# Kernel tuning notes

Hardware: AMD Instinct MI355X
Metric: run time of the kernel (lower is better)

Reference implementation:

```python
import jax, jax.numpy as jnp
import numpy as np

B, LB, LC, H = 8, 512, 128, 256
H2 = 2 * H
MIN_WS, N_WIN = 5, 4


def _highway(x, Wn, bn, Wl, bl, Wg, bg):
    # AllenNLP-style highway: per layer, gate * relu(nonlinear) + (1-gate) * linear
    # Wn/Wl/Wg: [L, D, D]; bn/bl/bg: [L, D]
    for i in range(Wn.shape[0]):
        g = jax.nn.sigmoid(x @ Wg[i] + bg[i])
        x = g * jax.nn.relu(x @ Wn[i] + bn[i]) + (1.0 - g) * (x @ Wl[i] + bl[i])
    return x


def _additive_scores(q, k, Wq, bq, Wk, v):
    # 'BilinearAttention' in the repo is additive: v^T tanh(Wq q + Wk k)
    # q: [..., Lq, D], k: [..., Lk, D] -> scores [..., Lq, Lk]
    wq = q @ Wq + bq
    uh = k @ Wk
    return jnp.tanh(wq[..., :, None, :] + uh[..., None, :, :]) @ v


def setup_inputs() -> dict:
    key = jax.random.key(0)
    ks = jax.random.split(key, 32)
    s2 = 1.0 / np.sqrt(H2)
    s1 = 1.0 / np.sqrt(H)
    d = {
        'b_enc_output': jax.random.normal(ks[0], (B, LB, H), jnp.float32),
        'c_enc_output': jax.random.normal(ks[1], (B, LC, H), jnp.float32),
        'c_state': jax.random.normal(ks[2], (B, 1, H), jnp.float32),
        'b_mask': jnp.ones((B, LB), bool),
        'c_mask': jnp.ones((B, LC), bool),
    }
    # b_highway / c_highway: 2 layers, each with nonlinear/linear/gate Linear(2H,2H)
    for pfx, base in (('bh', 3), ('ch', 9)):
        d[pfx + '_Wn'] = jax.random.normal(ks[base + 0], (2, H2, H2), jnp.float32) * s2
        d[pfx + '_bn'] = jnp.zeros((2, H2), jnp.float32)
        d[pfx + '_Wl'] = jax.random.normal(ks[base + 1], (2, H2, H2), jnp.float32) * s2
        d[pfx + '_bl'] = jnp.zeros((2, H2), jnp.float32)
        d[pfx + '_Wg'] = jax.random.normal(ks[base + 2], (2, H2, H2), jnp.float32) * s2
        d[pfx + '_bg'] = jnp.zeros((2, H2), jnp.float32)
    # match_attn (2H) and area_attn (H)
    d['m_Wq'] = jax.random.normal(ks[15], (H2, H2), jnp.float32) * s2
    d['m_bq'] = jnp.zeros((H2,), jnp.float32)
    d['m_Wk'] = jax.random.normal(ks[16], (H2, H2), jnp.float32) * s2
    d['m_v'] = jax.random.normal(ks[17], (H2,), jnp.float32) * s2
    d['a_Wq'] = jax.random.normal(ks[18], (H, H), jnp.float32) * s1
    d['a_bq'] = jnp.zeros((H,), jnp.float32)
    d['a_Wk'] = jax.random.normal(ks[19], (H, H), jnp.float32) * s1
    d['a_v'] = jax.random.normal(ks[20], (H,), jnp.float32) * s1
    return d


def reference(b_enc_output, c_enc_output, c_state,
              bh_Wn, bh_bn, bh_Wl, bh_bl, bh_Wg, bh_bg,
              ch_Wn, ch_bn, ch_Wl, ch_bl, ch_Wg, ch_bg,
              m_Wq, m_bq, m_Wk, m_v,
              a_Wq, a_bq, a_Wk, a_v,
              b_mask, c_mask):
    Bsz, Lb, Hd = b_enc_output.shape
    Lc = c_enc_output.shape[1]
    # match(): highway over [enc ; c_state]
    cs_b = jnp.broadcast_to(c_state, (Bsz, Lb, Hd))
    cs_c = jnp.broadcast_to(c_state, (Bsz, Lc, Hd))
    b = _highway(jnp.concatenate([b_enc_output, cs_b], -1), bh_Wn, bh_bn, bh_Wl, bh_bl, bh_Wg, bh_bg)
    c = _highway(jnp.concatenate([c_enc_output, cs_c], -1), ch_Wn, ch_bn, ch_Wl, ch_bl, ch_Wg, ch_bg)
    m = _additive_scores(b, c, m_Wq, m_bq, m_Wk, m_v)  # [B,Lb,Lc]
    m = jnp.where(c_mask[:, None, :], m, -jnp.inf)
    b_score = jnp.where(b_mask, jnp.max(m, axis=-1), 0.0)  # [B,Lb]
    # segments(): multi-scale sliding windows (unfold) + area attention
    q = c_state[:, :, None, :]  # [B,1,1,H]
    segs, scores = [], []
    for i in range(N_WIN):
        ws = MIN_WS * (i + 1)
        n_seg = (Lb - ws) // MIN_WS + 1
        idx = jnp.arange(n_seg)[:, None] * MIN_WS + jnp.arange(ws)[None, :]  # [n_seg, ws]
        bw = b_enc_output[:, idx, :]  # [B,n_seg,ws,H]
        attn = jax.nn.softmax(_additive_scores(q, bw, a_Wq, a_bq, a_Wk, a_v), axis=-1)  # [B,n_seg,1,ws]
        segs.append(jnp.einsum('bnqw,bnwh->bnh', attn, bw))
        scores.append(b_score[:, idx].sum(-1))  # [B,n_seg]
    segments = jnp.concatenate(segs, axis=1)          # [B,N,H]
    s_score = jax.nn.softmax(jnp.concatenate(scores, axis=1), axis=-1)  # [B,N]
    out = jnp.einsum('bn,bnh->bh', s_score, segments)[:, None, :]  # [B,1,H]
    return out, s_score, b_score
```

## Files before the change

kernel.cpp:

```cpp
#include <hip/hip_runtime.h>
#include <hip/hip_bf16.h>
#include <cstdint>
#include <cstddef>


typedef unsigned short ushort8 __attribute__((ext_vector_type(8)));
typedef float f32x4 __attribute__((ext_vector_type(4)));

__device__ __forceinline__ float fsigmoid(float x) { return 1.0f / (1.0f + __expf(-x)); }
__device__ __forceinline__ float ftanh(float x) {
  float e = __expf(2.0f * x);
  return 1.0f - 2.0f / (e + 1.0f);
}
__device__ __forceinline__ unsigned short f2bf(float x) {
  union { float f; unsigned u; } v; v.f = x;
  unsigned r = (v.u + 0x7FFFu + ((v.u >> 16) & 1u)) >> 16;
  return (unsigned short)r;
}
__device__ __forceinline__ f32x4 mfma_bf16(ushort8 a, ushort8 b, f32x4 c) {
  asm("v_mfma_f32_16x16x32_bf16 %0, %1, %2, %0" : "+v"(c) : "v"(a), "v"(b));
  return c;
}

struct WArg { const float* s[15]; };
__global__ __launch_bounds__(256) void prep_k(WArg wa, unsigned short* __restrict__ WT,
    const float* __restrict__ benc, const float* __restrict__ cenc,
    const float* __restrict__ cs,
    unsigned short* __restrict__ XB0, unsigned short* __restrict__ XC0,
    const float* __restrict__ aWq, const float* __restrict__ abq,
    float* __restrict__ wqa) {
  __shared__ float tile[64][65];
  const int blk = blockIdx.x, t = threadIdx.x;
  if (blk < 960) {
    const int mat = blk >> 6, q = blk & 63;
    const int Kd = (mat == 14) ? 256 : 512;
    const int k0 = (q >> 3) << 6, n0 = (q & 7) << 6;
    if (mat == 14 && (k0 >= 256 || n0 >= 256)) return;
    const float* __restrict__ S = wa.s[mat];
    unsigned short* __restrict__ D = WT + (size_t)mat * 262144;
#pragma unroll
    for (int i = 0; i < 16; ++i) {
      int id = i * 256 + t, r = id >> 6, c = id & 63;
      tile[r][c] = S[(size_t)(k0 + r) * Kd + (n0 + c)];
    }
    __syncthreads();
#pragma unroll
    for (int i = 0; i < 16; ++i) {
      int id = i * 256 + t, r = id >> 6, c = id & 63;
      D[(size_t)(n0 + r) * Kd + (k0 + c)] = f2bf(tile[c][r]);
    }
  } else if (blk < 3520) {
    const bool isB = blk < 3008;
    const float* enc = isB ? benc : cenc;
    unsigned short* out = isB ? XB0 : XC0;
    const int Lshift = isB ? 9 : 7;
    int i4 = (blk - (isB ? 960 : 3008)) * 256 + t;
    int row = i4 >> 7, c4 = (i4 & 127) << 2;
    float4 v;
    if (c4 < 256) v = *(const float4*)(enc + ((size_t)row << 8) + c4);
    else          v = *(const float4*)(cs + ((size_t)(row >> Lshift) << 8) + (c4 - 256));
    union { unsigned short u[4]; uint2 w; } o;
    o.u[0] = f2bf(v.x); o.u[1] = f2bf(v.y); o.u[2] = f2bf(v.z); o.u[3] = f2bf(v.w);
    *(uint2*)(out + ((size_t)row << 9) + c4) = o.w;
  } else {
    int b = blk - 3520, h = t;
    float acc = abq[h];
    for (int k = 0; k < 256; ++k) acc += cs[b * 256 + k] * aWq[k * 256 + h];
    wqa[b * 256 + h] = acc;
  }
}

template <int NB, int EPI>
__global__ __launch_bounds__(256) void mgemm_k(
    const unsigned short* __restrict__ A, int lda,
    const unsigned short* __restrict__ W0, const unsigned short* __restrict__ W1,
    const unsigned short* __restrict__ W2,
    const float* __restrict__ B0, const float* __restrict__ B1, const float* __restrict__ B2,
    void* __restrict__ Yv, int M, int N, int K) {
  __shared__ unsigned short sm[(1 + NB) * 4096];
  const int t = threadIdx.x;
  const int m0 = blockIdx.y * 64, n0 = blockIdx.x * 64;
  const int lane = t & 63, wid = t >> 6;
  const int wr = wid >> 1, wc = wid & 1;

  const int srow = t >> 3;
  const int cg = (t & 7) ^ (srow & 7);
  const unsigned short* Ag0 = A + (size_t)(m0 + srow) * lda + cg * 8;
  const unsigned short* Ag1 = A + (size_t)(m0 + 32 + srow) * lda + cg * 8;
  const unsigned short* Wp[3] = {W0, W1, W2};
  const unsigned short* Bg0[NB], * Bg1[NB];
#pragma unroll
  for (int p = 0; p < NB; ++p) {
    Bg0[p] = Wp[p] + (size_t)(n0 + srow) * K + cg * 8;
    Bg1[p] = Wp[p] + (size_t)(n0 + 32 + srow) * K + cg * 8;
  }
  const int d0 = t * 8, d1 = (256 + t) * 8;

  const int fl = lane & 15, lg = lane >> 4;
  int offA[2][2], offB[2][2];
#pragma unroll
  for (int f = 0; f < 2; ++f) {
    int ra = wr * 32 + f * 16 + fl;
    int rb = wc * 32 + f * 16 + fl;
#pragma unroll
    for (int ks = 0; ks < 2; ++ks) {
      offA[f][ks] = ra * 64 + ((((ks << 2) + lg) ^ (ra & 7)) << 3);
      offB[f][ks] = rb * 64 + ((((ks << 2) + lg) ^ (rb & 7)) << 3);
    }
  }

  f32x4 acc[NB][2][2];
#pragma unroll
  for (int p = 0; p < NB; ++p)
#pragma unroll
    for (int i = 0; i < 2; ++i)
#pragma unroll
      for (int j = 0; j < 2; ++j) acc[p][i][j] = (f32x4){0.f, 0.f, 0.f, 0.f};

  ushort8 ra0 = *(const ushort8*)Ag0, ra1 = *(const ushort8*)Ag1;
  ushort8 rb0[NB], rb1[NB];
#pragma unroll
  for (int p = 0; p < NB; ++p) { rb0[p] = *(const ushort8*)Bg0[p]; rb1[p] = *(const ushort8*)Bg1[p]; }

  for (int k0 = 0; k0 < K; k0 += 64) {
    __syncthreads();
    *(ushort8*)&sm[d0] = ra0;
    *(ushort8*)&sm[d1] = ra1;
#pragma unroll
    for (int p = 0; p < NB; ++p) {
      unsigned short* Bs = (unsigned short*)sm + (1 + p) * 4096;
      *(ushort8*)&Bs[d0] = rb0[p];
      *(ushort8*)&Bs[d1] = rb1[p];
    }
    __syncthreads();
    if (k0 + 64 < K) {
      ra0 = *(const ushort8*)(Ag0 + k0 + 64);
      ra1 = *(const ushort8*)(Ag1 + k0 + 64);
#pragma unroll
      for (int p = 0; p < NB; ++p) {
        rb0[p] = *(const ushort8*)(Bg0[p] + k0 + 64);
        rb1[p] = *(const ushort8*)(Bg1[p] + k0 + 64);
      }
    }
#pragma unroll
    for (int ks = 0; ks < 2; ++ks) {
      ushort8 a0 = *(const ushort8*)&sm[offA[0][ks]];
      ushort8 a1 = *(const ushort8*)&sm[offA[1][ks]];
#pragma unroll
      for (int p = 0; p < NB; ++p) {
        const unsigned short* Bs = (const unsigned short*)sm + (1 + p) * 4096;
        ushort8 b0 = *(const ushort8*)&Bs[offB[0][ks]];
        ushort8 b1 = *(const ushort8*)&Bs[offB[1][ks]];
        acc[p][0][0] = mfma_bf16(a0, b0, acc[p][0][0]);
        acc[p][0][1] = mfma_bf16(a0, b1, acc[p][0][1]);
        acc[p][1][0] = mfma_bf16(a1, b0, acc[p][1][0]);
        acc[p][1][1] = mfma_bf16(a1, b1, acc[p][1][1]);
      }
    }
  }
  asm volatile("s_nop 7\n\ts_nop 7" ::);

#pragma unroll
  for (int mf = 0; mf < 2; ++mf) {
#pragma unroll
    for (int nf = 0; nf < 2; ++nf) {
      const int col = n0 + wc * 32 + nf * 16 + fl;
      const int row0 = m0 + wr * 32 + mf * 16 + lg * 4;
      if constexpr (EPI == 1) {
        float bn = B0[col], bl = B1[col], bg = B2[col];
        unsigned short* Y = (unsigned short*)Yv;
#pragma unroll
        for (int e = 0; e < 4; ++e) {
          float nv = acc[0][mf][nf][e] + bn;
          float lv = acc[1][mf][nf][e] + bl;
          float gv = fsigmoid(acc[2][mf][nf][e] + bg);
          Y[(size_t)(row0 + e) * N + col] = f2bf(gv * fmaxf(nv, 0.f) + (1.f - gv) * lv);
        }
      } else if constexpr (EPI == 2) {
        float bb = B0[col];
        float* Y = (float*)Yv;
#pragma unroll
        for (int e = 0; e < 4; ++e)
          Y[(size_t)(row0 + e) * N + col] = __expf(2.0f * (acc[0][mf][nf][e] + bb));
      } else if constexpr (EPI == 3) {
        float* Y = (float*)Yv;
        f32x4 w;
#pragma unroll
        for (int e = 0; e < 4; ++e) w[e] = __expf(2.0f * acc[0][mf][nf][e]);
        *(f32x4*)(Y + (((size_t)(row0 >> 7)) << 16) + ((size_t)col << 7) + (row0 & 127)) = w;
      } else {
        float bb = B0 ? B0[col] : 0.f;
        float* Y = (float*)Yv;
#pragma unroll
        for (int e = 0; e < 4; ++e)
          Y[(size_t)(row0 + e) * N + col] = acc[0][mf][nf][e] + bb;
      }
    }
  }
}

__global__ __launch_bounds__(512) void mscore_k(const float* __restrict__ EW,
                                                const float* __restrict__ UHT,
                                                const float* __restrict__ mv,
                                                float* __restrict__ bscore) {
  __shared__ float eu[2][32 * 128];
  __shared__ float ews[8][512];
  __shared__ float vvs[512];
  const int t = threadIdx.x, lane = t & 63, wid = t >> 6;
  const int blk = blockIdx.x;
  const int b = blk >> 6;
  const int rg = (blk & 63) << 3;
  const int row = (b << 9) + rg + wid;
  const float* __restrict__ eub = UHT + ((size_t)b << 16);

#pragma unroll
  for (int i = 0; i < 2; ++i) {
    int f4 = i * 512 + t, r = f4 >> 7, c = (f4 & 127) << 2;
    *(float4*)&ews[r][c] = *(const float4*)(EW + (((size_t)((b << 9) + rg + r)) << 9) + c);
  }
  if (t < 128) *(float4*)&vvs[t << 2] = *(const float4*)(mv + (t << 2));

  float V = 0.f;
#pragma unroll
  for (int k = 0; k < 8; ++k) V += mv[lane + (k << 6)];
#pragma unroll
  for (int off = 32; off; off >>= 1) V += __shfl_xor(V, off);

  {
    float4 a = *(const float4*)(eub + (t << 2));
    float4 c = *(const float4*)(eub + ((512 + t) << 2));
    *(float4*)&eu[0][t << 2] = a;
    *(float4*)&eu[0][(512 + t) << 2] = c;
  }

  const int jg = lane & 31, hh = lane >> 5;
  f32x4 tj = (f32x4){0.f, 0.f, 0.f, 0.f};
  float e_reg[16], v_reg[16];

  for (int c = 0; c < 16; ++c) {
    __syncthreads();
    float4 na, nb;
    if (c < 15) {
      const float* src = eub + ((size_t)(c + 1) << 12);
      na = *(const float4*)(src + (t << 2));
      nb = *(const float4*)(src + ((512 + t) << 2));
    }
    const int hbase = (c << 5) + (hh << 4);
#pragma unroll
    for (int q = 0; q < 4; ++q) {
      *(float4*)&e_reg[q << 2] = *(const float4*)&ews[wid][hbase + (q << 2)];
      *(float4*)&v_reg[q << 2] = *(const float4*)&vvs[hbase + (q << 2)];
    }
    const float* eup = &eu[c & 1][(hh << 11) + (jg << 2)];
#pragma unroll
    for (int i = 0; i < 16; ++i) {
      float4 u = *(const float4*)(eup + (i << 7));
      float e = e_reg[i], vv = v_reg[i];
      tj.x += vv * __builtin_amdgcn_rcpf(__builtin_fmaf(e, u.x, 1.f));
      tj.y += vv * __builtin_amdgcn_rcpf(__builtin_fmaf(e, u.y, 1.f));
      tj.z += vv * __builtin_amdgcn_rcpf(__builtin_fmaf(e, u.z, 1.f));
      tj.w += vv * __builtin_amdgcn_rcpf(__builtin_fmaf(e, u.w, 1.f));
    }
    if (c < 15) {
      float* dst = &eu[(c + 1) & 1][0];
      *(float4*)&dst[t << 2] = na;
      *(float4*)&dst[(512 + t) << 2] = nb;
    }
  }

  tj.x += __shfl_xor(tj.x, 32);
  tj.y += __shfl_xor(tj.y, 32);
  tj.z += __shfl_xor(tj.z, 32);
  tj.w += __shfl_xor(tj.w, 32);
  float tm = fminf(fminf(tj.x, tj.y), fminf(tj.z, tj.w));
#pragma unroll
  for (int off = 16; off; off >>= 1) tm = fminf(tm, __shfl_xor(tm, off));
  if (lane == 0) bscore[row] = V - 2.f * tm;
}

__global__ __launch_bounds__(256) void tscore_k(const float* __restrict__ uha,
                                                const float* __restrict__ wqa,
                                                const float* __restrict__ av,
                                                float* __restrict__ t) {
  const int tid = threadIdx.x, lane = tid & 63, wid = tid >> 6;
  const int pos = blockIdx.x * 4 + wid;
  const int b = pos >> 9;
  const int h0 = lane << 2;
  float4 u = *(const float4*)(uha + (size_t)pos * 256 + h0);
  float4 w = *(const float4*)(wqa + b * 256 + h0);
  float4 v = *(const float4*)(av + h0);
  float s = ftanh(w.x + u.x) * v.x + ftanh(w.y + u.y) * v.y +
            ftanh(w.z + u.z) * v.z + ftanh(w.w + u.w) * v.w;
#pragma unroll
  for (int off = 32; off; off >>= 1) s += __shfl_xor(s, off);
  if (lane == 0) t[pos] = s;
}

__global__ __launch_bounds__(256) void seg_k(const float* __restrict__ t,
                                             const float* __restrict__ bscore,
                                             const float* __restrict__ benc,
                                             float* __restrict__ seg,
                                             float* __restrict__ sco) {
  const int s = blockIdx.x, b = blockIdx.y, h = threadIdx.x;
  int i, n;
  if (s < 102)      { i = 0; n = s; }
  else if (s < 203) { i = 1; n = s - 102; }
  else if (s < 303) { i = 2; n = s - 203; }
  else              { i = 3; n = s - 303; }
  const int ws = 5 * (i + 1), start = n * 5;
  const float* tb = t + b * 512 + start;
  float mx = -3.0e38f;
  for (int w = 0; w < ws; ++w) mx = fmaxf(mx, tb[w]);
  float sum = 0.f;
  for (int w = 0; w < ws; ++w) sum += __expf(tb[w] - mx);
  float inv = 1.f / sum;
  float acc = 0.f;
  for (int w = 0; w < ws; ++w)
    acc += __expf(tb[w] - mx) * benc[((size_t)(b * 512 + start + w)) * 256 + h];
  seg[((size_t)(b * 402 + s)) * 256 + h] = acc * inv;
  if (h == 0) {
    float ss = 0.f;
    const float* bs = bscore + b * 512 + start;
    for (int w = 0; w < ws; ++w) ss += bs[w];
    sco[b * 402 + s] = ss;
  }
}

__global__ __launch_bounds__(256) void final_k(const float* __restrict__ sco,
                                               const float* __restrict__ seg,
                                               float* __restrict__ dout) {
  const int b = blockIdx.x, tid = threadIdx.x, lane = tid & 63, wid = tid >> 6;
  __shared__ float sc[402];
  __shared__ float redm[4], reds[4];
  for (int s = tid; s < 402; s += 256) sc[s] = sco[b * 402 + s];
  __syncthreads();
  float m = -3.0e38f;
  for (int s = tid; s < 402; s += 256) m = fmaxf(m, sc[s]);
#pragma unroll
  for (int off = 32; off; off >>= 1) m = fmaxf(m, __shfl_xor(m, off));
  if (lane == 0) redm[wid] = m;
  __syncthreads();
  m = fmaxf(fmaxf(redm[0], redm[1]), fmaxf(redm[2], redm[3]));
  float p = 0.f;
  for (int s = tid; s < 402; s += 256) p += __expf(sc[s] - m);
#pragma unroll
  for (int off = 32; off; off >>= 1) p += __shfl_xor(p, off);
  if (lane == 0) reds[wid] = p;
  __syncthreads();
  float invS = 1.f / (reds[0] + reds[1] + reds[2] + reds[3]);
  for (int s = tid; s < 402; s += 256) {
    float pv = __expf(sc[s] - m) * invS;
    dout[2048 + b * 402 + s] = pv;
    sc[s] = pv;
  }
  __syncthreads();
  float acc = 0.f;
  for (int s = 0; s < 402; ++s)
    acc += sc[s] * seg[((size_t)(b * 402 + s)) * 256 + tid];
  dout[b * 256 + tid] = acc;
}

extern "C" void kernel_launch(void* const* d_in, const int* in_sizes, int n_in,
                              void* d_out, int out_size, void* d_ws, size_t ws_size,
                              hipStream_t stream) {
  const float* b_enc   = (const float*)d_in[0];
  const float* c_enc   = (const float*)d_in[1];
  const float* c_state = (const float*)d_in[2];
  const float* bh_Wn = (const float*)d_in[5];
  const float* bh_bn = (const float*)d_in[6];
  const float* bh_Wl = (const float*)d_in[7];
  const float* bh_bl = (const float*)d_in[8];
  const float* bh_Wg = (const float*)d_in[9];
  const float* bh_bg = (const float*)d_in[10];
  const float* ch_Wn = (const float*)d_in[11];
  const float* ch_bn = (const float*)d_in[12];
  const float* ch_Wl = (const float*)d_in[13];
  const float* ch_bl = (const float*)d_in[14];
  const float* ch_Wg = (const float*)d_in[15];
  const float* ch_bg = (const float*)d_in[16];
  const float* m_Wq  = (const float*)d_in[17];
  const float* m_bq  = (const float*)d_in[18];
  const float* m_Wk  = (const float*)d_in[19];
  const float* m_v   = (const float*)d_in[20];
  const float* a_Wq  = (const float*)d_in[21];
  const float* a_bq  = (const float*)d_in[22];
  const float* a_Wk  = (const float*)d_in[23];
  const float* a_v   = (const float*)d_in[24];

  uint8_t* base = (uint8_t*)d_ws;
  unsigned short* WT  = (unsigned short*)(base);
  unsigned short* WTa = WT + 14 * 262144;
  unsigned short* XB0 = (unsigned short*)(base + 7471104);
  unsigned short* XB1 = (unsigned short*)(base + 11665408);
  unsigned short* XC0 = (unsigned short*)(base + 15859712);
  unsigned short* XC1 = (unsigned short*)(base + 16908288);
  float* EW   = (float*)(base + 17956864);
  float* UHT  = (float*)(base + 26345472);
  float* UHA  = (float*)(base + 28442624);
  float* WQA  = (float*)(base + 32636928);
  float* T    = (float*)(base + 32645120);
  float* SEG  = (float*)(base + 32661504);
  float* SCO  = (float*)(base + 35954688);

  float* out = (float*)d_out;
  float* BSC = out + 5264;

  const int S = 262144;
  const int LW = 262144;

  WArg wa;
  wa.s[0] = bh_Wn; wa.s[1] = bh_Wn + LW;
  wa.s[2] = bh_Wl; wa.s[3] = bh_Wl + LW;
  wa.s[4] = bh_Wg; wa.s[5] = bh_Wg + LW;
  wa.s[6] = ch_Wn; wa.s[7] = ch_Wn + LW;
  wa.s[8] = ch_Wl; wa.s[9] = ch_Wl + LW;
  wa.s[10] = ch_Wg; wa.s[11] = ch_Wg + LW;
  wa.s[12] = m_Wq; wa.s[13] = m_Wk; wa.s[14] = a_Wk;

  prep_k<<<3528, 256, 0, stream>>>(wa, WT, b_enc, c_enc, c_state, XB0, XC0,
                                   a_Wq, a_bq, WQA);

  mgemm_k<1, 0><<<dim3(4, 64), 256, 0, stream>>>(XB0, 512, WTa, nullptr, nullptr,
      nullptr, nullptr, nullptr, UHA, 4096, 256, 256);

  mgemm_k<3, 1><<<dim3(8, 64), 256, 0, stream>>>(XB0, 512, WT, WT + 2 * S, WT + 4 * S,
      bh_bn, bh_bl, bh_bg, XB1, 4096, 512, 512);
  mgemm_k<3, 1><<<dim3(8, 64), 256, 0, stream>>>(XB1, 512, WT + S, WT + 3 * S, WT + 5 * S,
      bh_bn + 512, bh_bl + 512, bh_bg + 512, XB0, 4096, 512, 512);
  mgemm_k<3, 1><<<dim3(8, 16), 256, 0, stream>>>(XC0, 512, WT + 6 * S, WT + 8 * S, WT + 10 * S,
      ch_bn, ch_bl, ch_bg, XC1, 1024, 512, 512);
  mgemm_k<3, 1><<<dim3(8, 16), 256, 0, stream>>>(XC1, 512, WT + 7 * S, WT + 9 * S, WT + 11 * S,
      ch_bn + 512, ch_bl + 512, ch_bg + 512, XC0, 1024, 512, 512);

  mgemm_k<1, 2><<<dim3(8, 64), 256, 0, stream>>>(XB0, 512, WT + 12 * S, nullptr, nullptr,
      m_bq, nullptr, nullptr, EW, 4096, 512, 512);
  mgemm_k<1, 3><<<dim3(8, 16), 256, 0, stream>>>(XC0, 512, WT + 13 * S, nullptr, nullptr,
      nullptr, nullptr, nullptr, UHT, 1024, 512, 512);
  mscore_k<<<512, 512, 0, stream>>>(EW, UHT, m_v, BSC);

  tscore_k<<<1024, 256, 0, stream>>>(UHA, WQA, a_v, T);
  seg_k<<<dim3(402, 8), 256, 0, stream>>>(T, BSC, b_enc, SEG, SCO);
  final_k<<<8, 256, 0, stream>>>(SCO, SEG, out);
}
```

Before: 164.3 us.

## Batch independent GEMMs into grouped launches and fold tscore into GEMM kernel

The separate GEMM launches are merged into three grouped kernels. Each block dispatches, by its block index, to a job descriptor for the B-highway, C-highway, area-key or match-projection GEMM, and the tanh-score pass is appended as extra blocks of the last launch. mscore_k now uses 256 threads, each wave handling two rows so the staged UHT tile is reused across more work. This cuts kernel launches and lets small C-side GEMMs fill the GPU alongside the B-side ones. The cost is runtime branching on job fields, shared memory sized for the largest variant, and fewer waves per mscore block.

New measurement: 142.0 us. 13.6% less time.

```diff
diff --git a/kernel.cpp b/kernel.cpp
--- a/kernel.cpp
+++ b/kernel.cpp
@@ -70,24 +70,26 @@
   }
 }
 
-template <int NB, int EPI>
-__global__ __launch_bounds__(256) void mgemm_k(
-    const unsigned short* __restrict__ A, int lda,
-    const unsigned short* __restrict__ W0, const unsigned short* __restrict__ W1,
-    const unsigned short* __restrict__ W2,
-    const float* __restrict__ B0, const float* __restrict__ B1, const float* __restrict__ B2,
-    void* __restrict__ Yv, int M, int N, int K) {
-  __shared__ unsigned short sm[(1 + NB) * 4096];
-  const int t = threadIdx.x;
-  const int m0 = blockIdx.y * 64, n0 = blockIdx.x * 64;
+struct GJob {
+  const unsigned short* A; const unsigned short* W0;
+  const unsigned short* W1; const unsigned short* W2;
+  const float* B0; const float* B1; const float* B2;
+  void* Y; int lda, N, K, nbxs , epi, nb, blk0;
+};
+
+template <int NB>
+__device__ __forceinline__ void gemm_body(const GJob& j, int bx, int by,
+                                          unsigned short* sm, int t) {
+  const int m0 = by * 64, n0 = bx * 64;
   const int lane = t & 63, wid = t >> 6;
   const int wr = wid >> 1, wc = wid & 1;
+  const int N = j.N, K = j.K, lda = j.lda;
 
   const int srow = t >> 3;
   const int cg = (t & 7) ^ (srow & 7);
-  const unsigned short* Ag0 = A + (size_t)(m0 + srow) * lda + cg * 8;
-  const unsigned short* Ag1 = A + (size_t)(m0 + 32 + srow) * lda + cg * 8;
-  const unsigned short* Wp[3] = {W0, W1, W2};
+  const unsigned short* Ag0 = j.A + (size_t)(m0 + srow) * lda + cg * 8;
+  const unsigned short* Ag1 = j.A + (size_t)(m0 + 32 + srow) * lda + cg * 8;
+  const unsigned short* Wp[3] = {j.W0, j.W1, j.W2};
   const unsigned short* Bg0[NB], * Bg1[NB];
 #pragma unroll
   for (int p = 0; p < NB; ++p) {
@@ -115,7 +117,7 @@
 #pragma unroll
     for (int i = 0; i < 2; ++i)
 #pragma unroll
-      for (int j = 0; j < 2; ++j) acc[p][i][j] = (f32x4){0.f, 0.f, 0.f, 0.f};
+      for (int q = 0; q < 2; ++q) acc[p][i][q] = (f32x4){0.f, 0.f, 0.f, 0.f};
 
   ushort8 ra0 = *(const ushort8*)Ag0, ra1 = *(const ushort8*)Ag1;
   ushort8 rb0[NB], rb1[NB];
@@ -128,7 +130,7 @@
     *(ushort8*)&sm[d1] = ra1;
 #pragma unroll
     for (int p = 0; p < NB; ++p) {
-      unsigned short* Bs = (unsigned short*)sm + (1 + p) * 4096;
+      unsigned short* Bs = sm + (1 + p) * 4096;
       *(ushort8*)&Bs[d0] = rb0[p];
       *(ushort8*)&Bs[d1] = rb1[p];
     }
@@ -148,7 +150,7 @@
       ushort8 a1 = *(const ushort8*)&sm[offA[1][ks]];
 #pragma unroll
       for (int p = 0; p < NB; ++p) {
-        const unsigned short* Bs = (const unsigned short*)sm + (1 + p) * 4096;
+        const unsigned short* Bs = sm + (1 + p) * 4096;
         ushort8 b0 = *(const ushort8*)&Bs[offB[0][ks]];
         ushort8 b1 = *(const ushort8*)&Bs[offB[1][ks]];
         acc[p][0][0] = mfma_bf16(a0, b0, acc[p][0][0]);
@@ -166,9 +168,9 @@
     for (int nf = 0; nf < 2; ++nf) {
       const int col = n0 + wc * 32 + nf * 16 + fl;
       const int row0 = m0 + wr * 32 + mf * 16 + lg * 4;
-      if constexpr (EPI == 1) {
-        float bn = B0[col], bl = B1[col], bg = B2[col];
-        unsigned short* Y = (unsigned short*)Yv;
+      if constexpr (NB == 3) {
+        float bn = j.B0[col], bl = j.B1[col], bg = j.B2[col];
+        unsigned short* Y = (unsigned short*)j.Y;
 #pragma unroll
         for (int e = 0; e < 4; ++e) {
           float nv = acc[0][mf][nf][e] + bn;
@@ -176,30 +178,59 @@
           float gv = fsigmoid(acc[2][mf][nf][e] + bg);
           Y[(size_t)(row0 + e) * N + col] = f2bf(gv * fmaxf(nv, 0.f) + (1.f - gv) * lv);
         }
-      } else if constexpr (EPI == 2) {
-        float bb = B0[col];
-        float* Y = (float*)Yv;
-#pragma unroll
-        for (int e = 0; e < 4; ++e)
-          Y[(size_t)(row0 + e) * N + col] = __expf(2.0f * (acc[0][mf][nf][e] + bb));
-      } else if constexpr (EPI == 3) {
-        float* Y = (float*)Yv;
-        f32x4 w;
-#pragma unroll
-        for (int e = 0; e < 4; ++e) w[e] = __expf(2.0f * acc[0][mf][nf][e]);
-        *(f32x4*)(Y + (((size_t)(row0 >> 7)) << 16) + ((size_t)col << 7) + (row0 & 127)) = w;
       } else {
-        float bb = B0 ? B0[col] : 0.f;
-        float* Y = (float*)Yv;
-#pragma unroll
-        for (int e = 0; e < 4; ++e)
-          Y[(size_t)(row0 + e) * N + col] = acc[0][mf][nf][e] + bb;
+        float* Y = (float*)j.Y;
+        if (j.epi == 2) {
+          float bb = j.B0[col];
+#pragma unroll
+          for (int e = 0; e < 4; ++e)
+            Y[(size_t)(row0 + e) * N + col] = __expf(2.0f * (acc[0][mf][nf][e] + bb));
+        } else if (j.epi == 3) {
+          f32x4 w;
+#pragma unroll
+          for (int e = 0; e < 4; ++e) w[e] = __expf(2.0f * acc[0][mf][nf][e]);
+          *(f32x4*)(Y + (((size_t)(row0 >> 7)) << 16) + ((size_t)col << 7) + (row0 & 127)) = w;
+        } else {
+          float bb = j.B0 ? j.B0[col] : 0.f;
+#pragma unroll
+          for (int e = 0; e < 4; ++e)
+            Y[(size_t)(row0 + e) * N + col] = acc[0][mf][nf][e] + bb;
+        }
       }
     }
   }
 }
 
-__global__ __launch_bounds__(512) void mscore_k(const float* __restrict__ EW,
+__global__ __launch_bounds__(256) void mgemm3_k(GJob j0, GJob j1, GJob j2, int toff,
+    const float* __restrict__ uha, const float* __restrict__ wqa,
+    const float* __restrict__ av, float* __restrict__ tout) {
+  __shared__ unsigned short sm[4 * 4096];
+  const int blk = blockIdx.x, t = threadIdx.x;
+  if (blk >= toff) {
+    const int lane = t & 63, wid = t >> 6;
+    const int pos = (blk - toff) * 4 + wid;
+    const int b = pos >> 9;
+    const int h0 = lane << 2;
+    float4 u = *(const float4*)(uha + (size_t)pos * 256 + h0);
+    float4 w = *(const float4*)(wqa + b * 256 + h0);
+    float4 v = *(const float4*)(av + h0);
+    float s = ftanh(w.x + u.x) * v.x + ftanh(w.y + u.y) * v.y +
+              ftanh(w.z + u.z) * v.z + ftanh(w.w + u.w) * v.w;
+#pragma unroll
+    for (int off = 32; off; off >>= 1) s += __shfl_xor(s, off);
+    if (lane == 0) tout[pos] = s;
+    return;
+  }
+  GJob j = j0;
+  if (blk >= j1.blk0) j = j1;
+  if (blk >= j2.blk0) j = j2;
+  const int rel = blk - j.blk0;
+  const int bx = rel & ((1 << j.nbxs) - 1), by = rel >> j.nbxs;
+  if (j.nb == 3) gemm_body<3>(j, bx, by, sm, t);
+  else          gemm_body<1>(j, bx, by, sm, t);
+}
+
+__global__ __launch_bounds__(256) void mscore_k(const float* __restrict__ EW,
                                                 const float* __restrict__ UHT,
                                                 const float* __restrict__ mv,
                                                 float* __restrict__ bscore) {
@@ -208,15 +239,14 @@
   __shared__ float vvs[512];
   const int t = threadIdx.x, lane = t & 63, wid = t >> 6;
   const int blk = blockIdx.x;
-  const int b = blk >> 6;
-  const int rg = (blk & 63) << 3;
-  const int row = (b << 9) + rg + wid;
+  const int b = blk >> 6, g = blk & 63;
+  const int row0 = (b << 9) + (g << 3);
   const float* __restrict__ eub = UHT + ((size_t)b << 16);
 
 #pragma unroll
-  for (int i = 0; i < 2; ++i) {
-    int f4 = i * 512 + t, r = f4 >> 7, c = (f4 & 127) << 2;
-    *(float4*)&ews[r][c] = *(const float4*)(EW + (((size_t)((b << 9) + rg + r)) << 9) + c);
+  for (int q = 0; q < 4; ++q) {
+    int f4 = q * 256 + t, r = f4 >> 7, c4 = (f4 & 127) << 2;
+    *(float4*)&ews[r][c4] = *(const float4*)(EW + (((size_t)(row0 + r)) << 9) + c4);
   }
   if (t < 128) *(float4*)&vvs[t << 2] = *(const float4*)(mv + (t << 2));
 
@@ -226,74 +256,73 @@
 #pragma unroll
   for (int off = 32; off; off >>= 1) V += __shfl_xor(V, off);
 
-  {
-    float4 a = *(const float4*)(eub + (t << 2));
-    float4 c = *(const float4*)(eub + ((512 + t) << 2));
-    *(float4*)&eu[0][t << 2] = a;
-    *(float4*)&eu[0][(512 + t) << 2] = c;
+#pragma unroll
+  for (int q = 0; q < 4; ++q) {
+    int f4 = q * 256 + t;
+    *(float4*)&eu[0][f4 << 2] = *(const float4*)(eub + (f4 << 2));
   }
 
   const int jg = lane & 31, hh = lane >> 5;
-  f32x4 tj = (f32x4){0.f, 0.f, 0.f, 0.f};
-  float e_reg[16], v_reg[16];
+  const int lr = wid << 1;
+  f32x4 tj0 = (f32x4){0.f, 0.f, 0.f, 0.f};
+  f32x4 tj1 = (f32x4){0.f, 0.f, 0.f, 0.f};
+  float e0r[16], e1r[16], vr[16];
 
   for (int c = 0; c < 16; ++c) {
     __syncthreads();
-    float4 na, nb;
+    float4 pf0, pf1, pf2, pf3;
     if (c < 15) {
       const float* src = eub + ((size_t)(c + 1) << 12);
-      na = *(const float4*)(src + (t << 2));
-      nb = *(const float4*)(src + ((512 + t) << 2));
+      pf0 = *(const float4*)(src + (t << 2));
+      pf1 = *(const float4*)(src + ((256 + t) << 2));
+      pf2 = *(const float4*)(src + ((512 + t) << 2));
+      pf3 = *(const float4*)(src + ((768 + t) << 2));
     }
     const int hbase = (c << 5) + (hh << 4);
 #pragma unroll
     for (int q = 0; q < 4; ++q) {
-      *(float4*)&e_reg[q << 2] = *(const float4*)&ews[wid][hbase + (q << 2)];
-      *(float4*)&v_reg[q << 2] = *(const float4*)&vvs[hbase + (q << 2)];
-    }
-    const float* eup = &eu[c & 1][(hh << 11) + (jg << 2)];
+      *(float4*)&e0r[q << 2] = *(const float4*)&ews[lr][hbase + (q << 2)];
+      *(float4*)&e1r[q << 2] = *(const float4*)&ews[lr + 1][hbase + (q << 2)];
+      *(float4*)&vr[q << 2]  = *(const float4*)&vvs[hbase + (q << 2)];
+    }
+    const float* eup = &eu[c & 1][((hh << 4) << 7) + (jg << 2)];
 #pragma unroll
     for (int i = 0; i < 16; ++i) {
       float4 u = *(const float4*)(eup + (i << 7));
-      float e = e_reg[i], vv = v_reg[i];
-      tj.x += vv * __builtin_amdgcn_rcpf(__builtin_fmaf(e, u.x, 1.f));
-      tj.y += vv * __builtin_amdgcn_rcpf(__builtin_fmaf(e, u.y, 1.f));
-      tj.z += vv * __builtin_amdgcn_rcpf(__builtin_fmaf(e, u.z, 1.f));
-      tj.w += vv * __builtin_amdgcn_rcpf(__builtin_fmaf(e, u.w, 1.f));
+      float vv = vr[i], e0 = e0r[i], e1 = e1r[i];
+      tj0.x += vv * __builtin_amdgcn_rcpf(__builtin_fmaf(e0, u.x, 1.f));
+      tj0.y += vv * __builtin_amdgcn_rcpf(__builtin_fmaf(e0, u.y, 1.f));
+      tj0.z += vv * __builtin_amdgcn_rcpf(__builtin_fmaf(e0, u.z, 1.f));
+      tj0.w += vv * __builtin_amdgcn_rcpf(__builtin_fmaf(e0, u.w, 1.f));
+      tj1.x += vv * __builtin_amdgcn_rcpf(__builtin_fmaf(e1, u.x, 1.f));
+      tj1.y += vv * __builtin_amdgcn_rcpf(__builtin_fmaf(e1, u.y, 1.f));
+      tj1.z += vv * __builtin_amdgcn_rcpf(__builtin_fmaf(e1, u.z, 1.f));
+      tj1.w += vv * __builtin_amdgcn_rcpf(__builtin_fmaf(e1, u.w, 1.f));
     }
     if (c < 15) {
       float* dst = &eu[(c + 1) & 1][0];
-      *(float4*)&dst[t << 2] = na;
-      *(float4*)&dst[(512 + t) << 2] = nb;
-    }
-  }
-
-  tj.x += __shfl_xor(tj.x, 32);
-  tj.y += __shfl_xor(tj.y, 32);
-  tj.z += __shfl_xor(tj.z, 32);
-  tj.w += __shfl_xor(tj.w, 32);
-  float tm = fminf(fminf(tj.x, tj.y), fminf(tj.z, tj.w));
-#pragma unroll
-  for (int off = 16; off; off >>= 1) tm = fminf(tm, __shfl_xor(tm, off));
-  if (lane == 0) bscore[row] = V - 2.f * tm;
-}
-
-__global__ __launch_bounds__(256) void tscore_k(const float* __restrict__ uha,
-                                                const float* __restrict__ wqa,
-                                                const float* __restrict__ av,
-                                                float* __restrict__ t) {
-  const int tid = threadIdx.x, lane = tid & 63, wid = tid >> 6;
-  const int pos = blockIdx.x * 4 + wid;
-  const int b = pos >> 9;
-  const int h0 = lane << 2;
-  float4 u = *(const float4*)(uha + (size_t)pos * 256 + h0);
-  float4 w = *(const float4*)(wqa + b * 256 + h0);
-  float4 v = *(const float4*)(av + h0);
-  float s = ftanh(w.x + u.x) * v.x + ftanh(w.y + u.y) * v.y +
-            ftanh(w.z + u.z) * v.z + ftanh(w.w + u.w) * v.w;
-#pragma unroll
-  for (int off = 32; off; off >>= 1) s += __shfl_xor(s, off);
-  if (lane == 0) t[pos] = s;
+      *(float4*)&dst[t << 2] = pf0;
+      *(float4*)&dst[(256 + t) << 2] = pf1;
+      *(float4*)&dst[(512 + t) << 2] = pf2;
+      *(float4*)&dst[(768 + t) << 2] = pf3;
+    }
+  }
+
+  tj0.x += __shfl_xor(tj0.x, 32); tj0.y += __shfl_xor(tj0.y, 32);
+  tj0.z += __shfl_xor(tj0.z, 32); tj0.w += __shfl_xor(tj0.w, 32);
+  tj1.x += __shfl_xor(tj1.x, 32); tj1.y += __shfl_xor(tj1.y, 32);
+  tj1.z += __shfl_xor(tj1.z, 32); tj1.w += __shfl_xor(tj1.w, 32);
+  float m0 = fminf(fminf(tj0.x, tj0.y), fminf(tj0.z, tj0.w));
+  float m1 = fminf(fminf(tj1.x, tj1.y), fminf(tj1.z, tj1.w));
+#pragma unroll
+  for (int off = 16; off; off >>= 1) {
+    m0 = fminf(m0, __shfl_xor(m0, off));
+    m1 = fminf(m1, __shfl_xor(m1, off));
+  }
+  if (lane == 0) {
+    bscore[row0 + lr] = V - 2.f * m0;
+    bscore[row0 + lr + 1] = V - 2.f * m1;
+  }
 }
 
 __global__ __launch_bounds__(256) void seg_k(const float* __restrict__ t,
@@ -407,6 +436,7 @@
 
   const int S = 262144;
   const int LW = 262144;
+  const int SENT = 1 << 30;
 
   WArg wa;
   wa.s[0] = bh_Wn; wa.s[1] = bh_Wn + LW;
@@ -420,25 +450,33 @@
   prep_k<<<3528, 256, 0, stream>>>(wa, WT, b_enc, c_enc, c_state, XB0, XC0,
                                    a_Wq, a_bq, WQA);
 
-  mgemm_k<1, 0><<<dim3(4, 64), 256, 0, stream>>>(XB0, 512, WTa, nullptr, nullptr,
-      nullptr, nullptr, nullptr, UHA, 4096, 256, 256);
-
-  mgemm_k<3, 1><<<dim3(8, 64), 256, 0, stream>>>(XB0, 512, WT, WT + 2 * S, WT + 4 * S,
-      bh_bn, bh_bl, bh_bg, XB1, 4096, 512, 512);
-  mgemm_k<3, 1><<<dim3(8, 64), 256, 0, stream>>>(XB1, 512, WT + S, WT + 3 * S, WT + 5 * S,
-      bh_bn + 512, bh_bl + 512, bh_bg + 512, XB0, 4096, 512, 512);
-  mgemm_k<3, 1><<<dim3(8, 16), 256, 0, stream>>>(XC0, 512, WT + 6 * S, WT + 8 * S, WT + 10 * S,
-      ch_bn, ch_bl, ch_bg, XC1, 1024, 512, 512);
-  mgemm_k<3, 1><<<dim3(8, 16), 256, 0, stream>>>(XC1, 512, WT + 7 * S, WT + 9 * S, WT + 11 * S,
-      ch_bn + 512, ch_bl + 512, ch_bg + 512, XC0, 1024, 512, 512);
-
-  mgemm_k<1, 2><<<dim3(8, 64), 256, 0, stream>>>(XB0, 512, WT + 12 * S, nullptr, nullptr,
-      m_bq, nullptr, nullptr, EW, 4096, 512, 512);
-  mgemm_k<1, 3><<<dim3(8, 16), 256, 0, stream>>>(XC0, 512, WT + 13 * S, nullptr, nullptr,
-      nullptr, nullptr, nullptr, UHT, 1024, 512, 512);
-  mscore_k<<<512, 512, 0, stream>>>(EW, UHT, m_v, BSC);
-
-  tscore_k<<<1024, 256, 0, stream>>>(UHA, WQA, a_v, T);
+  {
+    GJob jb = {XB0, WT, WT + 2 * S, WT + 4 * S, bh_bn, bh_bl, bh_bg,
+               XB1, 512, 512, 512, 3, 1, 3, 0};
+    GJob jc = {XC0, WT + 6 * S, WT + 8 * S, WT + 10 * S, ch_bn, ch_bl, ch_bg,
+               XC1, 512, 512, 512, 3, 1, 3, 512};
+    GJob ja = {XB0, WTa, nullptr, nullptr, nullptr, nullptr, nullptr,
+               UHA, 512, 256, 256, 2, 0, 1, 640};
+    mgemm3_k<<<896, 256, 0, stream>>>(jb, jc, ja, 896, nullptr, nullptr, nullptr, nullptr);
+  }
+  {
+    GJob jb = {XB1, WT + S, WT + 3 * S, WT + 5 * S, bh_bn + 512, bh_bl + 512, bh_bg + 512,
+               XB0, 512, 512, 512, 3, 1, 3, 0};
+    GJob jc = {XC1, WT + 7 * S, WT + 9 * S, WT + 11 * S, ch_bn + 512, ch_bl + 512, ch_bg + 512,
+               XC0, 512, 512, 512, 3, 1, 3, 512};
+    GJob js = jc; js.blk0 = SENT;
+    mgemm3_k<<<640, 256, 0, stream>>>(jb, jc, js, 640, nullptr, nullptr, nullptr, nullptr);
+  }
+  {
+    GJob je = {XB0, WT + 12 * S, nullptr, nullptr, m_bq, nullptr, nullptr,
+               EW, 512, 512, 512, 3, 2, 1, 0};
+    GJob ju = {XC0, WT + 13 * S, nullptr, nullptr, nullptr, nullptr, nullptr,
+               UHT, 512, 512, 512, 3, 3, 1, 512};
+    GJob js = ju; js.blk0 = SENT;
+    mgemm3_k<<<1664, 256, 0, stream>>>(je, ju, js, 640, UHA, WQA, a_v, T);
+  }
+
+  mscore_k<<<512, 256, 0, stream>>>(EW, UHT, m_v, BSC);
   seg_k<<<dim3(402, 8), 256, 0, stream>>>(T, BSC, b_enc, SEG, SCO);
   final_k<<<8, 256, 0, stream>>>(SCO, SEG, out);
 }
```
